# Kernel tuning notes

Hardware: AMD Instinct MI355X
Metric: run time of the kernel (lower is better)

The kernel has to match this reference:

```python
import jax, jax.numpy as jnp
import numpy as np

HEADS = 4
PK = 32  # patch_kernel


def _starts(size, step, d):
    out = []
    for i in range(0, size + step - d, step):
        out.append(min(i, size - d))
    return np.asarray(out)


def dwconv3(x, w, b=None):
    # depthwise 3x3 conv, NCHW, weight (C,1,3,3)
    y = jax.lax.conv_general_dilated(
        x, w, window_strides=(1, 1), padding=((1, 1), (1, 1)),
        dimension_numbers=("NCHW", "OIHW", "NCHW"), feature_group_count=x.shape[1])
    if b is not None:
        y = y + b[None, :, None, None]
    return y


def conv1(x, w):
    # 1x1 conv as channel matmul, weight (O, C)
    return jnp.einsum("bchw,oc->bohw", x, w)


def partition(x, step, d):
    # overlapping windows, matching local_partition (i outer, j inner)
    b, c, h, w = x.shape
    sh = _starts(h, step, d)
    sw = _starts(w, step, d)
    ridx = sh[:, None] + np.arange(d)            # (nh, d)
    cidx = sw[:, None] + np.arange(d)            # (nw, d)
    xw = x[:, :, ridx, :]                        # (b, c, nh, d, w)
    xw = xw[:, :, :, :, cidx]                    # (b, c, nh, d, nw, d)
    xw = jnp.transpose(xw, (0, 2, 4, 1, 3, 5))   # (b, nh, nw, c, d, d)
    return xw.reshape(b, len(sh) * len(sw), c, d, d)


def reverse(shape, win, step, d):
    # overlap-add + count-based averaging, matching local_reverse
    b, c, h, w = shape
    sh = _starts(h, step, d)
    sw = _starts(w, step, d)
    nh, nw = len(sh), len(sw)
    ridx = (sh[:, None] + np.arange(d)).reshape(nh, 1, d, 1)
    cidx = (sw[:, None] + np.arange(d)).reshape(1, nw, 1, d)
    win6 = win.reshape(b, nh, nw, c, d, d).transpose(0, 3, 1, 2, 4, 5)  # (b,c,nh,nw,d,d)
    out = jnp.zeros(shape, win.dtype).at[:, :, ridx, cidx].add(win6)
    cnt = jnp.zeros((h, w), win.dtype).at[ridx, cidx].add(1.0)
    return out / cnt[None, None]


def setup_inputs() -> dict:
    key = jax.random.key(0)
    ks = jax.random.split(key, 9)
    b, dim, Hs, Hx = 2, 128, 62, 248
    s = 0.05
    return {
        "x": jax.random.normal(ks[0], (b, dim, Hx, Hx), jnp.float32),
        "sp": jax.random.normal(ks[1], (b, dim, Hs, Hs), jnp.float32),
        "w_pos": jax.random.normal(ks[2], (dim, 1, 3, 3), jnp.float32) * s,
        "b_pos": jax.random.normal(ks[3], (dim,), jnp.float32) * s,
        "w_q": jax.random.normal(ks[4], (dim, dim), jnp.float32) * s,
        "w_qdw": jax.random.normal(ks[5], (dim, 1, 3, 3), jnp.float32) * s,
        "w_kv": jax.random.normal(ks[6], (2 * dim, dim), jnp.float32) * s,
        "w_kvdw": jax.random.normal(ks[7], (2 * dim, 1, 3, 3), jnp.float32) * s,
        "w_out": jax.random.normal(ks[8], (dim, dim), jnp.float32) * s,
    }


def reference(x, sp, w_pos, b_pos, w_q, w_qdw, w_kv, w_kvdw, w_out):
    p1, p2 = PK, PK // 4               # 32, 8
    s1, s2 = p1 - p1 // 4, p2 - p2 // 4  # 24, 6
    x = x + dwconv3(x, w_pos, b_pos)
    sp = sp + dwconv3(sp, w_pos, b_pos)
    q = dwconv3(conv1(sp, w_q), w_qdw)      # (b, c, Hs, Ws)
    kv = dwconv3(conv1(x, w_kv), w_kvdw)    # (b, 2c, Hx, Wx)
    qw = partition(q, s2, p2)               # (b, n, c, 8, 8)
    kvw = partition(kv, s1, p1)             # (b, n, 2c, 32, 32)
    kw, vw = jnp.split(kvw, 2, axis=2)
    b, n, c = qw.shape[0], qw.shape[1], qw.shape[2]
    hd = c // HEADS

    def to_heads(t, d):  # 'b n (head c) dh dw -> (b n) head (dh dw) c'
        return t.reshape(b * n, HEADS, hd, d * d).transpose(0, 1, 3, 2)

    qh, kh, vh = to_heads(qw, p2), to_heads(kw, p1), to_heads(vw, p1)
    attn = jax.nn.softmax(jnp.einsum("bhqc,bhkc->bhqk", qh, kh) * (hd ** -0.5), axis=-1)
    out = jnp.einsum("bhqk,bhkc->bhqc", attn, vh)
    out = out.transpose(0, 1, 3, 2).reshape(b, n, c, p2, p2)
    out = reverse(sp.shape, out, s2, p2)
    return conv1(out, w_out)
```

## Files before the change

### kernel.cpp

```cpp
#include <hip/hip_runtime.h>
#include <cstdint>

#define HS 62
#define HX 248
#define HXW (HX * HX)
#define HSW (HS * HS)
#define HXP 256
#define HXWP (HX * HXP)

typedef __attribute__((ext_vector_type(8))) short bf16x8;
typedef __attribute__((ext_vector_type(4))) float f32x4;
typedef __attribute__((ext_vector_type(2))) float f32x2;

static __device__ __forceinline__ unsigned short f2bf(float f) {
  uint32_t u = __builtin_bit_cast(uint32_t, f);
  u += 0x7fff + ((u >> 16) & 1);
  return (unsigned short)(u >> 16);
}
static __device__ __forceinline__ float bf2f(unsigned short u) {
  uint32_t x = (uint32_t)u << 16;
  return __builtin_bit_cast(float, x);
}
static __device__ __forceinline__ float bflo(uint32_t u) {
  return __builtin_bit_cast(float, u << 16);
}
static __device__ __forceinline__ float bfhi(uint32_t u) {
  return __builtin_bit_cast(float, u & 0xffff0000u);
}

static __device__ __forceinline__ void pkfma(f32x2& acc, f32x2 a, f32x2 b) {
  asm("v_pk_fma_f32 %0, %1, %2, %0" : "+v"(acc) : "v"(a), "v"(b));
}
static __device__ __forceinline__ uint32_t cvtpk(float lo, float hi) {
  uint32_t r;
  asm("v_cvt_pk_bf16_f32 %0, %1, %2" : "=v"(r) : "v"(lo), "v"(hi));
  return r;
}
static __device__ __forceinline__ f32x2 unp(uint32_t u) {
  f32x2 r;
  r.x = __builtin_bit_cast(float, u << 16);
  r.y = __builtin_bit_cast(float, u & 0xffff0000u);
  return r;
}

__global__ void dwconv3_kernel(const float* __restrict__ x, const float* __restrict__ w,
                               const float* __restrict__ bias, float* __restrict__ y,
                               int C, int H, int W, int total, int residual) {
  int i = blockIdx.x * 256 + threadIdx.x;
  if (i >= total) return;
  int wx = i % W;
  int t = i / W;
  int hy = t % H;
  int bc = t / H;
  int c = bc % C;
  const float* xb = x + (size_t)bc * H * W;
  const float* wc = w + c * 9;
  float s = bias ? bias[c] : 0.0f;
  for (int di = -1; di <= 1; di++) {
    int h2 = hy + di;
    if (h2 < 0 || h2 >= H) continue;
    for (int dj = -1; dj <= 1; dj++) {
      int w2 = wx + dj;
      if (w2 < 0 || w2 >= W) continue;
      s += xb[(size_t)h2 * W + w2] * wc[(di + 1) * 3 + (dj + 1)];
    }
  }
  if (residual) s += xb[(size_t)hy * W + wx];
  y[i] = s;
}

__global__ __launch_bounds__(256) void dwconv8x2_bf16_kernel(
    const float* __restrict__ x, const float* __restrict__ w,
    const float* __restrict__ bias, unsigned short* __restrict__ y, int total) {
  int i = blockIdx.x * 256 + threadIdx.x;
  if (i >= total) return;
  int wq = (i % 31) * 8;
  int t = i / 31;
  int hp = t % 124;
  int bc = t / 124;
  int c = bc & 127;
  int hy = hp * 2;
  const float* xb = x + (size_t)bc * HXW;
  const float* wc = w + c * 9;
  float bv = bias[c];

  float rm1[10], r0[10], r1[10], r2[10];
  auto loadrow = [&](int h2, float (&r)[10]) {
    const float* row = xb + (size_t)h2 * HX + wq;
    float4 a = *(const float4*)row;
    float4 b2 = *(const float4*)(row + 4);
    r[1] = a.x;  r[2] = a.y;  r[3] = a.z;  r[4] = a.w;
    r[5] = b2.x; r[6] = b2.y; r[7] = b2.z; r[8] = b2.w;
    r[0] = (wq > 0) ? row[-1] : 0.0f;
    r[9] = (wq + 8 < HX) ? row[8] : 0.0f;
  };
  loadrow((hy > 0) ? hy - 1 : 0, rm1);
  loadrow(hy, r0);
  loadrow(hy + 1, r1);
  loadrow((hy + 2 < HX) ? hy + 2 : HX - 1, r2);
  if (hp == 0) {
#pragma unroll
    for (int k = 0; k < 10; k++) rm1[k] = 0.0f;
  }
  if (hp == 123) {
#pragma unroll
    for (int k = 0; k < 10; k++) r2[k] = 0.0f;
  }

  float w0 = wc[0], w1 = wc[1], w2 = wc[2];
  float w3 = wc[3], w4 = wc[4], w5 = wc[5];
  float w6 = wc[6], w7 = wc[7], w8 = wc[8];

  float o0[8], o1[8];
#pragma unroll
  for (int k = 0; k < 8; k++) {
    float s = bv;
    s += w0 * rm1[k]; s += w1 * rm1[k + 1]; s += w2 * rm1[k + 2];
    s += w3 * r0[k];  s += w4 * r0[k + 1];  s += w5 * r0[k + 2];
    s += w6 * r1[k];  s += w7 * r1[k + 1];  s += w8 * r1[k + 2];
    o0[k] = s + r0[k + 1];
    float u = bv;
    u += w0 * r0[k]; u += w1 * r0[k + 1]; u += w2 * r0[k + 2];
    u += w3 * r1[k]; u += w4 * r1[k + 1]; u += w5 * r1[k + 2];
    u += w6 * r2[k]; u += w7 * r2[k + 1]; u += w8 * r2[k + 2];
    o1[k] = u + r1[k + 1];
  }
  uint4 d0, d1;
  d0.x = cvtpk(o0[0], o0[1]); d0.y = cvtpk(o0[2], o0[3]);
  d0.z = cvtpk(o0[4], o0[5]); d0.w = cvtpk(o0[6], o0[7]);
  d1.x = cvtpk(o1[0], o1[1]); d1.y = cvtpk(o1[2], o1[3]);
  d1.z = cvtpk(o1[4], o1[5]); d1.w = cvtpk(o1[6], o1[7]);
  unsigned short* yb = y + (size_t)bc * HXW + (size_t)hy * HX + wq;
  *(uint4*)yb = d0;
  *(uint4*)(yb + HX) = d1;
}

__global__ void pack_wfrag_kernel(const float* __restrict__ w_kv,
                                  unsigned short* __restrict__ wf) {
  int i = blockIdx.x * 256 + threadIdx.x;
  if (i >= 4096) return;
  int lane = i & 63;
  int f = i >> 6;
  int hq = f >> 4, ot = (f >> 2) & 3, kb = f & 3;
  int l15 = lane & 15, quad = lane >> 4;
  const float* src = w_kv + (size_t)(hq * 64 + ot * 16 + l15) * 128 + kb * 32 + quad * 8;
  unsigned short* dst = wf + (size_t)i * 8;
#pragma unroll
  for (int j = 0; j < 8; j++) dst[j] = f2bf(src[j]);
}

__global__ void dwconv_q_kernel(const float* __restrict__ x, const float* __restrict__ w,
                                unsigned short* __restrict__ qn, int total) {
  int i = blockIdx.x * 256 + threadIdx.x;
  if (i >= total) return;
  int wx = i % HS;
  int t = i / HS;
  int hy = t % HS;
  int bc = t / HS;
  int c = bc & 127;
  int b = bc >> 7;
  const float* xb = x + (size_t)bc * HSW;
  const float* wc = w + c * 9;
  float s = 0.0f;
  for (int di = -1; di <= 1; di++) {
    int h2 = hy + di;
    if (h2 < 0 || h2 >= HS) continue;
    for (int dj = -1; dj <= 1; dj++) {
      int w2 = wx + dj;
      if (w2 < 0 || w2 >= HS) continue;
      s += xb[(size_t)h2 * HS + w2] * wc[(di + 1) * 3 + (dj + 1)];
    }
  }
  qn[((size_t)(b * HSW + hy * HS + wx)) * 128 + c] = f2bf(s * 0.17677669529663688f);
}

__global__ __launch_bounds__(256) void conv1_kv_mfma_kernel(
    const unsigned short* __restrict__ xpb,
    const unsigned short* __restrict__ wf,
    unsigned short* __restrict__ y) {
  int b = blockIdx.y;
  int p0 = blockIdx.x * 64;
  int tid = threadIdx.x;
  int wave = tid >> 6, lane = tid & 63, quad = lane >> 4, l15 = lane & 15;
  __shared__ __align__(16) unsigned short bufA[64 * 136];

  {
    int pxg = (tid & 7) * 8;
    int c0 = (tid >> 3) * 4;
    const unsigned short* src = xpb + ((size_t)(b * 128 + c0)) * HXW + p0 + pxg;
    uint4 r0 = *(const uint4*)(src);
    uint4 r1 = *(const uint4*)(src + (size_t)HXW);
    uint4 r2 = *(const uint4*)(src + 2 * (size_t)HXW);
    uint4 r3 = *(const uint4*)(src + 3 * (size_t)HXW);
    const uint32_t* q0 = (const uint32_t*)&r0;
    const uint32_t* q1 = (const uint32_t*)&r1;
    const uint32_t* q2 = (const uint32_t*)&r2;
    const uint32_t* q3 = (const uint32_t*)&r3;
    int swz = ((pxg >> 3) & 7) << 3;
    int cs = c0 ^ swz;
#pragma unroll
    for (int p = 0; p < 4; p++) {
      uint32_t d0 = q0[p], d1 = q1[p], d2 = q2[p], d3 = q3[p];
      uint2 wlo, whi;
      wlo.x = (d0 & 0xffffu) | (d1 << 16);
      wlo.y = (d2 & 0xffffu) | (d3 << 16);
      whi.x = (d0 >> 16) | (d1 & 0xffff0000u);
      whi.y = (d2 >> 16) | (d3 & 0xffff0000u);
      *(uint2*)&bufA[(pxg + 2 * p) * 136 + cs] = wlo;
      *(uint2*)&bufA[(pxg + 2 * p + 1) * 136 + cs] = whi;
    }
  }
  __syncthreads();

  bf16x8 A[4];
  {
    int px = wave * 16 + l15;
    int swz = ((px >> 3) & 7) << 3;
#pragma unroll
    for (int kb = 0; kb < 4; kb++)
      A[kb] = __builtin_bit_cast(bf16x8,
          *(const uint4*)&bufA[px * 136 + ((kb * 32 + quad * 8) ^ swz)]);
  }

  const f32x4 zf = {0.f, 0.f, 0.f, 0.f};
  const uint4* wfu = (const uint4*)wf;
  uint4 Bc[4], Bn[4];
  {
    const uint4* fb = wfu + lane;
    Bc[0] = fb[0]; Bc[1] = fb[64]; Bc[2] = fb[128]; Bc[3] = fb[192];
  }
  int orow = wave * 16 + quad * 4;
#pragma unroll 1
  for (int h = 0; h < 2; h++) {
#pragma unroll
    for (int tt = 0; tt < 8; tt++) {
      int t = h * 8 + tt;
      if (t < 15) {
        const uint4* fb = wfu + (size_t)(t + 1) * 256 + lane;
        Bn[0] = fb[0]; Bn[1] = fb[64]; Bn[2] = fb[128]; Bn[3] = fb[192];
      }
      f32x4 D = zf;
      D = __builtin_amdgcn_mfma_f32_16x16x32_bf16(A[0], __builtin_bit_cast(bf16x8, Bc[0]), D, 0, 0, 0);
      D = __builtin_amdgcn_mfma_f32_16x16x32_bf16(A[1], __builtin_bit_cast(bf16x8, Bc[1]), D, 0, 0, 0);
      D = __builtin_amdgcn_mfma_f32_16x16x32_bf16(A[2], __builtin_bit_cast(bf16x8, Bc[2]), D, 0, 0, 0);
      D = __builtin_amdgcn_mfma_f32_16x16x32_bf16(A[3], __builtin_bit_cast(bf16x8, Bc[3]), D, 0, 0, 0);
      int col = tt * 16 + l15;
#pragma unroll
      for (int r = 0; r < 4; r++) {
        int row = orow + r;
        bufA[row * 136 + (col ^ (((row >> 3) & 7) << 3))] = f2bf(D[r]);
      }
      if (t < 15) {
#pragma unroll
        for (int k = 0; k < 4; k++) Bc[k] = Bn[k];
      }
    }
    __syncthreads();
    {
      int px = tid >> 2, og = (tid & 3) * 32;
      int swz = ((px >> 3) & 7) << 3;
      uint4* dstp = (uint4*)(y + ((size_t)b * HXW + p0 + px) * 256 + h * 128 + og);
#pragma unroll
      for (int j = 0; j < 4; j++)
        dstp[j] = *(const uint4*)&bufA[px * 136 + ((og + j * 8) ^ swz)];
    }
    __syncthreads();
  }
}

template <bool VT, bool VB>
static __device__ __forceinline__ void dwkv_rowpair(
    const unsigned short* __restrict__ rm1, const unsigned short* __restrict__ r0,
    const unsigned short* __restrict__ r1, const unsigned short* __restrict__ r2,
    const f32x2 (&wp)[9], int px0, f32x2 (&a0)[8], f32x2 (&a1)[8]) {
  const f32x2 z2 = {0.f, 0.f};
#pragma unroll
  for (int p = 0; p < 8; p++) { a0[p] = z2; a1[p] = z2; }
#pragma unroll
  for (int j = 0; j < 10; j++) {
    int xcol = px0 - 1 + j;
    int xc = xcol;
    if (j == 0) xc = (xcol < 0) ? 0 : xcol;
    if (j == 9) xc = (xcol > HX - 1) ? HX - 1 : xcol;
    size_t off = (size_t)xc * 256;
    uint32_t um1 = 0, u0, u1, u2 = 0;
    u0 = *(const uint32_t*)(r0 + off);
    u1 = *(const uint32_t*)(r1 + off);
    if constexpr (VT) um1 = *(const uint32_t*)(rm1 + off);
    if constexpr (VB) u2 = *(const uint32_t*)(r2 + off);
    if (j == 0 || j == 9) {
      bool oob = (j == 0) ? (xcol < 0) : (xcol > HX - 1);
      if (oob) { um1 = 0u; u0 = 0u; u1 = 0u; u2 = 0u; }
    }
    f32x2 dm1, d0 = unp(u0), d1 = unp(u1), d2;
    if constexpr (VT) dm1 = unp(um1);
    if constexpr (VB) d2 = unp(u2);
    if (j <= 7) {
      if constexpr (VT) pkfma(a0[j], wp[0], dm1);
      pkfma(a0[j], wp[3], d0);
      pkfma(a0[j], wp[6], d1);
      pkfma(a1[j], wp[0], d0);
      pkfma(a1[j], wp[3], d1);
      if constexpr (VB) pkfma(a1[j], wp[6], d2);
    }
    if (j >= 1 && j <= 8) {
      if constexpr (VT) pkfma(a0[j - 1], wp[1], dm1);
      pkfma(a0[j - 1], wp[4], d0);
      pkfma(a0[j - 1], wp[7], d1);
      pkfma(a1[j - 1], wp[1], d0);
      pkfma(a1[j - 1], wp[4], d1);
      if constexpr (VB) pkfma(a1[j - 1], wp[7], d2);
    }
    if (j >= 2) {
      if constexpr (VT) pkfma(a0[j - 2], wp[2], dm1);
      pkfma(a0[j - 2], wp[5], d0);
      pkfma(a0[j - 2], wp[8], d1);
      pkfma(a1[j - 2], wp[2], d0);
      pkfma(a1[j - 2], wp[5], d1);
      if constexpr (VB) pkfma(a1[j - 2], wp[8], d2);
    }
  }
}

#define VTS 72
#define VTROW (128 * VTS + 16)

__global__ __launch_bounds__(512) __attribute__((amdgpu_waves_per_eu(4)))
void dwconv_kv_kernel(const unsigned short* __restrict__ tkv,
                      const float* __restrict__ w,
                      unsigned short* __restrict__ kT,
                      unsigned short* __restrict__ vv) {
  int fid = blockIdx.x;
  int xcd = fid & 7, slot = fid >> 3;
  int gi = xcd * 62 + slot;
  int strip = gi / 124;
  int g = gi % 124;
  int b = blockIdx.y;
  int x0 = strip * 64;
  int tid = threadIdx.x;
  int cl = tid & 127;
  int pg = tid >> 7;
  int ch0 = cl * 2;
  int hy0 = g * 2;

  f32x2 wp[9];
#pragma unroll
  for (int t = 0; t < 9; t++) {
    wp[t].x = w[ch0 * 9 + t];
    wp[t].y = w[(ch0 + 1) * 9 + t];
  }

  __shared__ __align__(16) unsigned short vt[2 * VTROW];

  const unsigned short* r0 = tkv + (size_t)b * HXW * 256 + (size_t)hy0 * (HX * 256) + ch0;
  const unsigned short* r1 = r0 + HX * 256;
  const unsigned short* rm1 = r0 - HX * 256;
  const unsigned short* r2 = r1 + HX * 256;
  bool isK = (cl < 64);
  int c0 = ch0 - 128;

#pragma unroll 1
  for (int half = 0; half < 2; half++) {
    int px0 = x0 + pg * 16 + half * 8;
    if (px0 < HX) {
      f32x2 a0[8], a1[8];
      if (g == 0)        dwkv_rowpair<false, true >(rm1, r0, r1, r2, wp, px0, a0, a1);
      else if (g == 123) dwkv_rowpair<true,  false>(rm1, r0, r1, r2, wp, px0, a0, a1);
      else               dwkv_rowpair<true,  true >(rm1, r0, r1, r2, wp, px0, a0, a1);

      if (isK) {
        unsigned short* kb0 = kT + ((size_t)b * HXW + (size_t)hy0 * HX + px0) * 128 + ch0;
        unsigned short* kb1 = kb0 + (size_t)HX * 128;
#pragma unroll
        for (int p = 0; p < 8; p++) {
          *(uint32_t*)(kb0 + (size_t)p * 128) = cvtpk(a0[p].x, a0[p].y);
          *(uint32_t*)(kb1 + (size_t)p * 128) = cvtpk(a1[p].x, a1[p].y);
        }
      } else {
        int pxr = pg * 16 + half * 8;
        unsigned short* v0 = vt + c0 * VTS + pxr;
        unsigned short* v1 = v0 + VTS;
        uint2 d;
        d.x = cvtpk(a0[0].x, a0[1].x); d.y = cvtpk(a0[2].x, a0[3].x);
        *(uint2*)(v0) = d;
        d.x = cvtpk(a0[4].x, a0[5].x); d.y = cvtpk(a0[6].x, a0[7].x);
        *(uint2*)(v0 + 4) = d;
        d.x = cvtpk(a0[0].y, a0[1].y); d.y = cvtpk(a0[2].y, a0[3].y);
        *(uint2*)(v1) = d;
        d.x = cvtpk(a0[4].y, a0[5].y); d.y = cvtpk(a0[6].y, a0[7].y);
        *(uint2*)(v1 + 4) = d;
        d.x = cvtpk(a1[0].x, a1[1].x); d.y = cvtpk(a1[2].x, a1[3].x);
        *(uint2*)(v0 + VTROW) = d;
        d.x = cvtpk(a1[4].x, a1[5].x); d.y = cvtpk(a1[6].x, a1[7].x);
        *(uint2*)(v0 + VTROW + 4) = d;
        d.x = cvtpk(a1[0].y, a1[1].y); d.y = cvtpk(a1[2].y, a1[3].y);
        *(uint2*)(v1 + VTROW) = d;
        d.x = cvtpk(a1[4].y, a1[5].y); d.y = cvtpk(a1[6].y, a1[7].y);
        *(uint2*)(v1 + VTROW + 4) = d;
      }
    }
  }
  __syncthreads();
  {
    int ch = tid >> 2;
    int row = (tid >> 1) & 1;
    int ph = (tid & 1) * 32;
    const unsigned short* srcv = vt + row * VTROW + ch * VTS + ph;
    unsigned short* dst = vv + (size_t)(b * 128 + ch) * HXWP + (size_t)(hy0 + row) * HXP + x0 + ph;
#pragma unroll
    for (int j = 0; j < 4; j++)
      *(uint4*)(dst + j * 8) = *(const uint4*)(srcv + j * 8);
  }
}

template <int O>
__global__ __launch_bounds__(256) void conv1_kernel(const float* __restrict__ x,
                                                    const float* __restrict__ w,
                                                    float* __restrict__ y, int HW) {
  constexpr int K = 128;
  constexpr int BK = 32;
  __shared__ __align__(16) float ws_s[BK][64];
  __shared__ __align__(16) float xs_s[BK][64];
  int b = blockIdx.z;
  int o0 = blockIdx.y * 64;
  int p0 = blockIdx.x * 64;
  const float* xb = x + (size_t)b * K * HW;
  int tx = threadIdx.x & 15;
  int ty = threadIdx.x >> 4;
  float acc[4][4] = {};
  int lo = threadIdx.x >> 2;
  int lk = (threadIdx.x & 3) * 8;
  int lc = threadIdx.x >> 3;
  int lp = (threadIdx.x & 7) * 8;

  for (int k0 = 0; k0 < K; k0 += BK) {
    __syncthreads();
    {
      const float* wp = w + (size_t)(o0 + lo) * K + k0 + lk;
      float4 a = *(const float4*)wp;
      float4 bq = *(const float4*)(wp + 4);
      ws_s[lk + 0][lo] = a.x;  ws_s[lk + 1][lo] = a.y;
      ws_s[lk + 2][lo] = a.z;  ws_s[lk + 3][lo] = a.w;
      ws_s[lk + 4][lo] = bq.x; ws_s[lk + 5][lo] = bq.y;
      ws_s[lk + 6][lo] = bq.z; ws_s[lk + 7][lo] = bq.w;
    }
    {
      int p = p0 + lp;
      const float* xp = xb + (size_t)(k0 + lc) * HW;
      float4 a, bq;
      if (p + 7 < HW) {
        a = *(const float4*)(xp + p);
        bq = *(const float4*)(xp + p + 4);
      } else {
        float tv[8];
#pragma unroll
        for (int j = 0; j < 8; j++) tv[j] = (p + j < HW) ? xp[p + j] : 0.0f;
        a = make_float4(tv[0], tv[1], tv[2], tv[3]);
        bq = make_float4(tv[4], tv[5], tv[6], tv[7]);
      }
      *(float4*)&xs_s[lc][lp] = a;
      *(float4*)&xs_s[lc][lp + 4] = bq;
    }
    __syncthreads();
#pragma unroll
    for (int k = 0; k < BK; k++) {
      float4 wv = *(const float4*)&ws_s[k][ty * 4];
      float4 xv = *(const float4*)&xs_s[k][tx * 4];
      acc[0][0] += wv.x * xv.x; acc[0][1] += wv.x * xv.y; acc[0][2] += wv.x * xv.z; acc[0][3] += wv.x * xv.w;
      acc[1][0] += wv.y * xv.x; acc[1][1] += wv.y * xv.y; acc[1][2] += wv.y * xv.z; acc[1][3] += wv.y * xv.w;
      acc[2][0] += wv.z * xv.x; acc[2][1] += wv.z * xv.y; acc[2][2] += wv.z * xv.z; acc[2][3] += wv.z * xv.w;
      acc[3][0] += wv.w * xv.x; acc[3][1] += wv.w * xv.y; acc[3][2] += wv.w * xv.z; acc[3][3] += wv.w * xv.w;
    }
  }
  int p = p0 + tx * 4;
  float* yb = y + (size_t)b * O * HW + (size_t)(o0 + ty * 4) * HW;
#pragma unroll
  for (int j = 0; j < 4; j++) {
    float* yr = yb + (size_t)j * HW + p;
    if (p + 3 < HW) {
      *(float4*)yr = make_float4(acc[j][0], acc[j][1], acc[j][2], acc[j][3]);
    } else {
#pragma unroll
      for (int e = 0; e < 4; e++) if (p + e < HW) yr[e] = acc[j][e];
    }
  }
}

__global__ __launch_bounds__(256) void attn_mfma_kernel(
    const unsigned short* __restrict__ qn,
    const unsigned short* __restrict__ kT,
    const unsigned short* __restrict__ vp,
    float* __restrict__ o) {
  int fid = blockIdx.x;
  int xcd = fid & 7, slot = fid >> 3;
  int lin = xcd * 100 + slot;
  int n = lin % 100;
  int bh = lin / 100;
  int h = bh & 3, b = bh >> 2;
  int wi = n / 10, wj = n % 10;
  int wave = threadIdx.x >> 6;
  int oct = wave;
  int lane = threadIdx.x & 63;
  int quad = lane >> 4;
  int l15 = lane & 15;
  int y0 = 24 * wi, x0 = 24 * wj;

  __shared__ __align__(16) unsigned short lds[16896];
  unsigned short* Pw = lds + wave * 2560;

  bf16x8 QB[4];
#pragma unroll
  for (int nt = 0; nt < 4; nt++) {
    int qq = nt * 16 + l15;
    int qy = 6 * wi + (qq >> 3), qx = 6 * wj + (qq & 7);
    QB[nt] = __builtin_bit_cast(bf16x8,
        *(const uint4*)(qn + ((size_t)(b * HSW + qy * HS + qx)) * 128 + h * 32 + quad * 8));
  }

  f32x4 Oacc[2][4];
#pragma unroll
  for (int a = 0; a < 2; a++)
#pragma unroll
    for (int c = 0; c < 4; c++) Oacc[a][c] = f32x4{0.f, 0.f, 0.f, 0.f};
  float lsum[4] = {0.f, 0.f, 0.f, 0.f};

  const unsigned short* kb = kT + (size_t)b * HXW * 128 + h * 32;
  const unsigned short* vb = vp + ((size_t)(b * 128 + h * 32)) * HXWP;
  const f32x4 zf = {0.f, 0.f, 0.f, 0.f};

#define LOADROW(r, K0, K1, V0, V1)                                              \
  {                                                                             \
    int y = y0 + (r);                                                           \
    const unsigned short* krow = kb + ((size_t)(y * HX + x0)) * 128;            \
    K0 = *(const uint4*)(krow + (size_t)l15 * 128 + quad * 8);                  \
    K1 = *(const uint4*)(krow + (size_t)(16 + l15) * 128 + quad * 8);           \
    const unsigned short* vrow = vb + (size_t)y * HXP + x0 + quad * 8;          \
    V0 = *(const uint4*)(vrow + (size_t)l15 * HXWP);                            \
    V1 = *(const uint4*)(vrow + (size_t)(16 + l15) * HXWP);                     \
  }

  auto compute = [&](uint4 k0, uint4 k1, uint4 v0, uint4 v1) {
    bf16x8 KA0 = __builtin_bit_cast(bf16x8, k0);
    bf16x8 KA1 = __builtin_bit_cast(bf16x8, k1);
    bf16x8 VA0 = __builtin_bit_cast(bf16x8, v0);
    bf16x8 VA1 = __builtin_bit_cast(bf16x8, v1);
    f32x4 S[2][4];
#pragma unroll
    for (int nt = 0; nt < 4; nt++) {
      S[0][nt] = __builtin_amdgcn_mfma_f32_16x16x32_bf16(KA0, QB[nt], zf, 0, 0, 0);
      S[1][nt] = __builtin_amdgcn_mfma_f32_16x16x32_bf16(KA1, QB[nt], zf, 0, 0, 0);
    }
#pragma unroll
    for (int nt = 0; nt < 4; nt++) {
      float pv[2][4];
      float cs = 0.f;
#pragma unroll
      for (int mt = 0; mt < 2; mt++)
#pragma unroll
        for (int r = 0; r < 4; r++) {
          pv[mt][r] = __expf(S[mt][nt][r]);
          cs += pv[mt][r];
        }
      lsum[nt] += cs;
#pragma unroll
      for (int mt = 0; mt < 2; mt++) {
        uint2 d;
        d.x = (uint32_t)f2bf(pv[mt][0]) | ((uint32_t)f2bf(pv[mt][1]) << 16);
        d.y = (uint32_t)f2bf(pv[mt][2]) | ((uint32_t)f2bf(pv[mt][3]) << 16);
        *(uint2*)(Pw + (16 * nt + l15) * 40 + 16 * mt + quad * 4) = d;
      }
    }
#pragma unroll
    for (int nt = 0; nt < 4; nt++) {
      bf16x8 PB = __builtin_bit_cast(bf16x8, *(const uint4*)(Pw + (16 * nt + l15) * 40 + quad * 8));
      Oacc[0][nt] = __builtin_amdgcn_mfma_f32_16x16x32_bf16(VA0, PB, Oacc[0][nt], 0, 0, 0);
      Oacc[1][nt] = __builtin_amdgcn_mfma_f32_16x16x32_bf16(VA1, PB, Oacc[1][nt], 0, 0, 0);
    }
  };

  int rbase = oct * 8;
  uint4 kA0, kA1, vA0, vA1, kB0, kB1, vB0, vB1;
  LOADROW(rbase + 0, kA0, kA1, vA0, vA1);
  LOADROW(rbase + 1, kB0, kB1, vB0, vB1);
#pragma unroll 1
  for (int r = 0; r < 8; r += 2) {
    compute(kA0, kA1, vA0, vA1);
    {
      int rn = (r + 2 < 8) ? (r + 2) : 6;
      LOADROW(rbase + rn, kA0, kA1, vA0, vA1);
    }
    compute(kB0, kB1, vB0, vB1);
    {
      int rn = (r + 3 < 8) ? (r + 3) : 7;
      LOADROW(rbase + rn, kB0, kB1, vB0, vB1);
    }
  }
#undef LOADROW

#pragma unroll
  for (int nt = 0; nt < 4; nt++) {
    lsum[nt] += __shfl_xor(lsum[nt], 16, 64);
    lsum[nt] += __shfl_xor(lsum[nt], 32, 64);
  }

  float* mO = (float*)lds;
  float* mL = (float*)(lds + 16384);
  __syncthreads();
#pragma unroll
  for (int mt = 0; mt < 2; mt++)
#pragma unroll
    for (int nt = 0; nt < 4; nt++)
#pragma unroll
      for (int r = 0; r < 4; r++)
        mO[oct * 2048 + (16 * mt + quad * 4 + r) * 64 + 16 * nt + l15] = Oacc[mt][nt][r];
  if (quad == 0) {
#pragma unroll
    for (int nt = 0; nt < 4; nt++) mL[oct * 64 + nt * 16 + l15] = lsum[nt];
  }
  __syncthreads();
  {
    int q = threadIdx.x & 63;
    int cg = threadIdx.x >> 6;
    float inv = 1.0f / (mL[q] + mL[64 + q] + mL[128 + q] + mL[192 + q]);
    float* ob = o + (((size_t)(b * 100 + n)) * 128 + h * 32 + cg * 8) * 64 + q;
#pragma unroll
    for (int e = 0; e < 8; e++) {
      int ch = cg * 8 + e;
      float s = mO[ch * 64 + q] + mO[2048 + ch * 64 + q] +
                mO[4096 + ch * 64 + q] + mO[6144 + ch * 64 + q];
      ob[(size_t)e * 64] = s * inv;
    }
  }
}

__global__ void reverse_kernel(const float* __restrict__ win, float* __restrict__ out) {
  int i = blockIdx.x * 256 + threadIdx.x;
  const int total = 2 * 128 * HSW;
  if (i >= total) return;
  int x = i % HS;
  int t = i / HS;
  int y = t % HS;
  t /= HS;
  int c = t % 128;
  int b = t / 128;
  int wi0 = (y >= 7) ? (y - 2) / 6 : 0;
  int wi1 = min(9, y / 6);
  int wj0 = (x >= 7) ? (x - 2) / 6 : 0;
  int wj1 = min(9, x / 6);
  float s = 0.0f;
  for (int wi = wi0; wi <= wi1; wi++)
    for (int wj = wj0; wj <= wj1; wj++) {
      int di = y - 6 * wi, dj = x - 6 * wj;
      s += win[(((size_t)(b * 100 + wi * 10 + wj)) * 128 + c) * 64 + di * 8 + dj];
    }
  float cnt = (float)((wi1 - wi0 + 1) * (wj1 - wj0 + 1));
  out[i] = s / cnt;
}

extern "C" void kernel_launch(void* const* d_in, const int* in_sizes, int n_in,
                              void* d_out, int out_size, void* d_ws, size_t ws_size,
                              hipStream_t stream) {
  const float* x      = (const float*)d_in[0];
  const float* sp     = (const float*)d_in[1];
  const float* w_pos  = (const float*)d_in[2];
  const float* b_pos  = (const float*)d_in[3];
  const float* w_q    = (const float*)d_in[4];
  const float* w_qdw  = (const float*)d_in[5];
  const float* w_kv   = (const float*)d_in[6];
  const float* w_kvdw = (const float*)d_in[7];
  const float* w_out  = (const float*)d_in[8];
  float* out = (float*)d_out;

  const size_t N_x   = (size_t)2 * 128 * HXW;
  const size_t N_vp  = (size_t)2 * 128 * HXWP;
  const size_t N_s   = (size_t)2 * 128 * HSW;
  const size_t N_att = (size_t)2 * 100 * 128 * 64;

  float* ws = (float*)d_ws;
  unsigned short* xpb = (unsigned short*)ws;
  unsigned short* kT  = (unsigned short*)ws;
  unsigned short* vv  = kT + N_x;
  unsigned short* tkv = vv + N_vp;
  float* att = (float*)tkv;
  float* rev = att + N_att;
  float* spp = (float*)(tkv + 2 * N_x);
  float* tq  = spp + N_s;
  unsigned short* qn  = (unsigned short*)(tq + N_s);
  unsigned short* wkb = qn + N_s;
  (void)ws_size; (void)in_sizes; (void)n_in; (void)out_size;

  pack_wfrag_kernel<<<16, 256, 0, stream>>>(w_kv, wkb);
  {
    int total = 2 * 128 * 124 * 31;
    dwconv8x2_bf16_kernel<<<(total + 255) / 256, 256, 0, stream>>>(x, w_pos, b_pos, xpb, total);
  }
  {
    int total = (int)N_s;
    dwconv3_kernel<<<(total + 255) / 256, 256, 0, stream>>>(sp, w_pos, b_pos, spp, 128, HS, HS, total, 1);
  }
  {
    int HW = HSW;
    dim3 grid((HW + 63) / 64, 2, 2);
    conv1_kernel<128><<<grid, 256, 0, stream>>>(spp, w_q, tq, HW);
  }
  {
    int total = (int)N_s;
    dwconv_q_kernel<<<(total + 255) / 256, 256, 0, stream>>>(tq, w_qdw, qn, total);
  }
  {
    dim3 grid(HXW / 64, 2);
    conv1_kv_mfma_kernel<<<grid, 256, 0, stream>>>(xpb, wkb, tkv);
  }
  {
    dim3 grid(496, 2);
    dwconv_kv_kernel<<<grid, 512, 0, stream>>>(tkv, w_kvdw, kT, vv);
  }
  {
    attn_mfma_kernel<<<800, 256, 0, stream>>>(qn, kT, vv, att);
  }
  {
    int total = (int)N_s;
    reverse_kernel<<<(total + 255) / 256, 256, 0, stream>>>(att, rev);
  }
  {
    int HW = HSW;
    dim3 grid((HW + 63) / 64, 2, 2);
    conv1_kernel<128><<<grid, 256, 0, stream>>>(rev, w_out, out, HW);
  }
}
```

Measured before the change: 258.5 us.

## Fuse positional depthwise conv into kv 1x1 MFMA kernel prologue

Removes the separate depthwise 3x3 positional conv kernel that wrote a bf16 intermediate of x. The kv 1x1 MFMA kernel now reads fp32 x directly, computes the 3x3 conv plus bias and residual for its 64-pixel by 128-channel tile, and packs the results into shared memory. This saves one launch and a full write and read of the intermediate. In exchange, the 3-row halo is read from global memory per tile (about three fp32 reads per pixel instead of one bf16 read), and the 62x62 path now runs after this larger kernel in stream order.

```diff
diff --git a/kernel.cpp b/kernel.cpp
--- a/kernel.cpp
+++ b/kernel.cpp
@@ -69,72 +69,6 @@
   y[i] = s;
 }
 
-__global__ __launch_bounds__(256) void dwconv8x2_bf16_kernel(
-    const float* __restrict__ x, const float* __restrict__ w,
-    const float* __restrict__ bias, unsigned short* __restrict__ y, int total) {
-  int i = blockIdx.x * 256 + threadIdx.x;
-  if (i >= total) return;
-  int wq = (i % 31) * 8;
-  int t = i / 31;
-  int hp = t % 124;
-  int bc = t / 124;
-  int c = bc & 127;
-  int hy = hp * 2;
-  const float* xb = x + (size_t)bc * HXW;
-  const float* wc = w + c * 9;
-  float bv = bias[c];
-
-  float rm1[10], r0[10], r1[10], r2[10];
-  auto loadrow = [&](int h2, float (&r)[10]) {
-    const float* row = xb + (size_t)h2 * HX + wq;
-    float4 a = *(const float4*)row;
-    float4 b2 = *(const float4*)(row + 4);
-    r[1] = a.x;  r[2] = a.y;  r[3] = a.z;  r[4] = a.w;
-    r[5] = b2.x; r[6] = b2.y; r[7] = b2.z; r[8] = b2.w;
-    r[0] = (wq > 0) ? row[-1] : 0.0f;
-    r[9] = (wq + 8 < HX) ? row[8] : 0.0f;
-  };
-  loadrow((hy > 0) ? hy - 1 : 0, rm1);
-  loadrow(hy, r0);
-  loadrow(hy + 1, r1);
-  loadrow((hy + 2 < HX) ? hy + 2 : HX - 1, r2);
-  if (hp == 0) {
-#pragma unroll
-    for (int k = 0; k < 10; k++) rm1[k] = 0.0f;
-  }
-  if (hp == 123) {
-#pragma unroll
-    for (int k = 0; k < 10; k++) r2[k] = 0.0f;
-  }
-
-  float w0 = wc[0], w1 = wc[1], w2 = wc[2];
-  float w3 = wc[3], w4 = wc[4], w5 = wc[5];
-  float w6 = wc[6], w7 = wc[7], w8 = wc[8];
-
-  float o0[8], o1[8];
-#pragma unroll
-  for (int k = 0; k < 8; k++) {
-    float s = bv;
-    s += w0 * rm1[k]; s += w1 * rm1[k + 1]; s += w2 * rm1[k + 2];
-    s += w3 * r0[k];  s += w4 * r0[k + 1];  s += w5 * r0[k + 2];
-    s += w6 * r1[k];  s += w7 * r1[k + 1];  s += w8 * r1[k + 2];
-    o0[k] = s + r0[k + 1];
-    float u = bv;
-    u += w0 * r0[k]; u += w1 * r0[k + 1]; u += w2 * r0[k + 2];
-    u += w3 * r1[k]; u += w4 * r1[k + 1]; u += w5 * r1[k + 2];
-    u += w6 * r2[k]; u += w7 * r2[k + 1]; u += w8 * r2[k + 2];
-    o1[k] = u + r1[k + 1];
-  }
-  uint4 d0, d1;
-  d0.x = cvtpk(o0[0], o0[1]); d0.y = cvtpk(o0[2], o0[3]);
-  d0.z = cvtpk(o0[4], o0[5]); d0.w = cvtpk(o0[6], o0[7]);
-  d1.x = cvtpk(o1[0], o1[1]); d1.y = cvtpk(o1[2], o1[3]);
-  d1.z = cvtpk(o1[4], o1[5]); d1.w = cvtpk(o1[6], o1[7]);
-  unsigned short* yb = y + (size_t)bc * HXW + (size_t)hy * HX + wq;
-  *(uint4*)yb = d0;
-  *(uint4*)(yb + HX) = d1;
-}
-
 __global__ void pack_wfrag_kernel(const float* __restrict__ w_kv,
                                   unsigned short* __restrict__ wf) {
   int i = blockIdx.x * 256 + threadIdx.x;
@@ -174,8 +108,10 @@
   qn[((size_t)(b * HSW + hy * HS + wx)) * 128 + c] = f2bf(s * 0.17677669529663688f);
 }
 
-__global__ __launch_bounds__(256) void conv1_kv_mfma_kernel(
-    const unsigned short* __restrict__ xpb,
+__global__ __launch_bounds__(256) void dwconv1_fused_kernel(
+    const float* __restrict__ x,
+    const float* __restrict__ wpos,
+    const float* __restrict__ bias,
     const unsigned short* __restrict__ wf,
     unsigned short* __restrict__ y) {
   int b = blockIdx.y;
@@ -187,28 +123,63 @@
   {
     int pxg = (tid & 7) * 8;
     int c0 = (tid >> 3) * 4;
-    const unsigned short* src = xpb + ((size_t)(b * 128 + c0)) * HXW + p0 + pxg;
-    uint4 r0 = *(const uint4*)(src);
-    uint4 r1 = *(const uint4*)(src + (size_t)HXW);
-    uint4 r2 = *(const uint4*)(src + 2 * (size_t)HXW);
-    uint4 r3 = *(const uint4*)(src + 3 * (size_t)HXW);
-    const uint32_t* q0 = (const uint32_t*)&r0;
-    const uint32_t* q1 = (const uint32_t*)&r1;
-    const uint32_t* q2 = (const uint32_t*)&r2;
-    const uint32_t* q3 = (const uint32_t*)&r3;
-    int swz = ((pxg >> 3) & 7) << 3;
-    int cs = c0 ^ swz;
-#pragma unroll
-    for (int p = 0; p < 4; p++) {
-      uint32_t d0 = q0[p], d1 = q1[p], d2 = q2[p], d3 = q3[p];
-      uint2 wlo, whi;
-      wlo.x = (d0 & 0xffffu) | (d1 << 16);
-      wlo.y = (d2 & 0xffffu) | (d3 << 16);
-      whi.x = (d0 >> 16) | (d1 & 0xffff0000u);
-      whi.y = (d2 >> 16) | (d3 & 0xffff0000u);
-      *(uint2*)&bufA[(pxg + 2 * p) * 136 + cs] = wlo;
-      *(uint2*)&bufA[(pxg + 2 * p + 1) * 136 + cs] = whi;
-    }
+    int flat = p0 + pxg;
+    int row = flat / HX;
+    int col = flat % HX;
+    int swz = (tid & 7) << 3;
+    bool top = (row == 0), bot = (row == HX - 1);
+    int rm = top ? 0 : row - 1;
+    int rp = bot ? HX - 1 : row + 1;
+    int csbase = c0 ^ swz;
+
+    auto do2 = [&](int c) {
+      const float* xb0 = x + ((size_t)(b * 128 + c)) * HXW;
+      const float* xb1 = xb0 + HXW;
+      const float* wc0 = wpos + c * 9;
+      const float* wc1 = wc0 + 9;
+      float bv0 = bias[c], bv1 = bias[c + 1];
+      float A0[10], B0[10], C0[10], A1[10], B1[10], C1[10];
+      auto loadrow = [&](const float* xb, int h2, float (&r)[10]) {
+        const float* rowp = xb + (size_t)h2 * HX + col;
+        float4 a = *(const float4*)rowp;
+        float4 b2 = *(const float4*)(rowp + 4);
+        r[1] = a.x;  r[2] = a.y;  r[3] = a.z;  r[4] = a.w;
+        r[5] = b2.x; r[6] = b2.y; r[7] = b2.z; r[8] = b2.w;
+        r[0] = (col > 0) ? rowp[-1] : 0.0f;
+        r[9] = (col + 8 < HX) ? rowp[8] : 0.0f;
+      };
+      loadrow(xb0, rm, A0); loadrow(xb0, row, B0); loadrow(xb0, rp, C0);
+      loadrow(xb1, rm, A1); loadrow(xb1, row, B1); loadrow(xb1, rp, C1);
+      if (top) {
+#pragma unroll
+        for (int k = 0; k < 10; k++) { A0[k] = 0.0f; A1[k] = 0.0f; }
+      }
+      if (bot) {
+#pragma unroll
+        for (int k = 0; k < 10; k++) { C0[k] = 0.0f; C1[k] = 0.0f; }
+      }
+      float u0 = wc0[0], u1 = wc0[1], u2 = wc0[2], u3 = wc0[3], u4 = wc0[4],
+            u5 = wc0[5], u6 = wc0[6], u7 = wc0[7], u8 = wc0[8];
+      float v0 = wc1[0], v1 = wc1[1], v2 = wc1[2], v3 = wc1[3], v4 = wc1[4],
+            v5 = wc1[5], v6 = wc1[6], v7 = wc1[7], v8 = wc1[8];
+      int cs = csbase + (c - c0);
+#pragma unroll
+      for (int k = 0; k < 8; k++) {
+        float s = bv0;
+        s += u0 * A0[k]; s += u1 * A0[k + 1]; s += u2 * A0[k + 2];
+        s += u3 * B0[k]; s += u4 * B0[k + 1]; s += u5 * B0[k + 2];
+        s += u6 * C0[k]; s += u7 * C0[k + 1]; s += u8 * C0[k + 2];
+        float o0 = s + B0[k + 1];
+        float t2 = bv1;
+        t2 += v0 * A1[k]; t2 += v1 * A1[k + 1]; t2 += v2 * A1[k + 2];
+        t2 += v3 * B1[k]; t2 += v4 * B1[k + 1]; t2 += v5 * B1[k + 2];
+        t2 += v6 * C1[k]; t2 += v7 * C1[k + 1]; t2 += v8 * C1[k + 2];
+        float o1 = t2 + B1[k + 1];
+        *(uint32_t*)&bufA[(pxg + k) * 136 + cs] = cvtpk(o0, o1);
+      }
+    };
+    do2(c0);
+    do2(c0 + 2);
   }
   __syncthreads();
 
@@ -677,7 +648,6 @@
   const size_t N_att = (size_t)2 * 100 * 128 * 64;
 
   float* ws = (float*)d_ws;
-  unsigned short* xpb = (unsigned short*)ws;
   unsigned short* kT  = (unsigned short*)ws;
   unsigned short* vv  = kT + N_x;
   unsigned short* tkv = vv + N_vp;
@@ -691,8 +661,8 @@
 
   pack_wfrag_kernel<<<16, 256, 0, stream>>>(w_kv, wkb);
   {
-    int total = 2 * 128 * 124 * 31;
-    dwconv8x2_bf16_kernel<<<(total + 255) / 256, 256, 0, stream>>>(x, w_pos, b_pos, xpb, total);
+    dim3 grid(HXW / 64, 2);
+    dwconv1_fused_kernel<<<grid, 256, 0, stream>>>(x, w_pos, b_pos, wkb, tkv);
   }
   {
     int total = (int)N_s;
@@ -708,10 +678,6 @@
     dwconv_q_kernel<<<(total + 255) / 256, 256, 0, stream>>>(tq, w_qdw, qn, total);
   }
   {
-    dim3 grid(HXW / 64, 2);
-    conv1_kv_mfma_kernel<<<grid, 256, 0, stream>>>(xpb, wkb, tkv);
-  }
-  {
     dim3 grid(496, 2);
     dwconv_kv_kernel<<<grid, 512, 0, stream>>>(tkv, w_kvdw, kT, vv);
   }
```

Measured after the change: 266.4 us. +3.1%, slower.
